# Performance work log

Hardware: AMD Instinct MI355X
Metric: run time of the kernel (lower is better)

## Reference

```python
import jax, jax.numpy as jnp
import numpy as np

B, T, C, H = 2, 2048, 2048, 16
DH = C // H  # 128
INNER = 4 * C  # 8192
EPS = 1e-5


def _ln(x, w, b):
    mu = jnp.mean(x, axis=-1, keepdims=True)
    var = jnp.mean((x - mu) ** 2, axis=-1, keepdims=True)
    return (x - mu) * jax.lax.rsqrt(var + EPS) * w + b


def _apply_rotary(x, cos, sin):
    # x: [B,H,T,DH]; cos/sin: [T,DH//2] broadcast over B,H
    x1 = x[..., ::2]
    x2 = x[..., 1::2]
    r = jnp.stack([x1 * cos - x2 * sin, x1 * sin + x2 * cos], axis=-1)
    return r.reshape(r.shape[:-2] + (-1,))


def setup_inputs() -> dict:
    key = jax.random.key(0)
    ks = jax.random.split(key, 8)
    std = 0.02
    x = jax.random.normal(ks[0], (B, T, C), dtype=jnp.float32)
    # RoPE tables
    inv_freq = 1.0 / (10000.0 ** (np.arange(0, DH, 2, dtype=np.float32) / DH))
    ang = np.arange(T, dtype=np.float32)[:, None] * inv_freq[None, :]  # [T, DH//2]
    cos = jnp.asarray(np.cos(ang))
    sin = jnp.asarray(np.sin(ang))
    return {
        "x": x,
        "cos": cos,
        "sin": sin,
        "ln1_w": jnp.ones((C,), jnp.float32),
        "ln1_b": jnp.zeros((C,), jnp.float32),
        "ln2_w": jnp.ones((C,), jnp.float32),
        "ln2_b": jnp.zeros((C,), jnp.float32),
        "W_qkv": jax.random.normal(ks[1], (C, 3 * C), jnp.float32) * std,
        "W_o": jax.random.normal(ks[2], (C, C), jnp.float32) * std,
        "W1": jax.random.normal(ks[3], (C, INNER), jnp.float32) * std,
        "W2": jax.random.normal(ks[4], (C, INNER), jnp.float32) * std,
        "W3": jax.random.normal(ks[5], (INNER, C), jnp.float32) * std,
    }


def reference(x, cos, sin, ln1_w, ln1_b, ln2_w, ln2_b, W_qkv, W_o, W1, W2, W3):
    # --- attention sub-block (pre-LN) ---
    a = _ln(x, ln1_w, ln1_b)
    qkv = a @ W_qkv  # [B,T,3C]
    q, k, v = jnp.split(qkv, 3, axis=-1)
    q = q.reshape(B, T, H, DH).transpose(0, 2, 1, 3)  # [B,H,T,DH]
    k = k.reshape(B, T, H, DH).transpose(0, 2, 1, 3)
    v = v.reshape(B, T, H, DH).transpose(0, 2, 1, 3)
    q = _apply_rotary(q, cos, sin)
    k = _apply_rotary(k, cos, sin)
    scores = jnp.einsum("bhtd,bhsd->bhts", q, k) / jnp.sqrt(jnp.float32(DH))
    mask = jnp.triu(jnp.full((T, T), -jnp.inf, dtype=scores.dtype), k=1)
    scores = scores + mask
    attn = jax.nn.softmax(scores, axis=-1)
    y = jnp.einsum("bhts,bhsd->bhtd", attn, v)
    y = y.transpose(0, 2, 1, 3).reshape(B, T, C) @ W_o
    x = x + y
    # --- SwiGLU MLP sub-block (pre-LN) ---
    h = _ln(x, ln2_w, ln2_b)
    m = (jax.nn.silu(h @ W1) * (h @ W2)) @ W3
    return x + m
```

## Files before the change

kernel.cpp:

```cpp
#include <hip/hip_runtime.h>
#include <hip/hip_bf16.h>
#include <cstdint>

#define DEVINL __device__ __forceinline__

using f32x4  = __attribute__((ext_vector_type(4))) float;
using short8 = __attribute__((ext_vector_type(8))) short;
using short4v = __attribute__((ext_vector_type(4))) short;

DEVINL float bf2f(__hip_bfloat16 h){ return __bfloat162float(h); }
DEVINL __hip_bfloat16 f2bf(float f){ return __float2bfloat16(f); }
DEVINL short bfbits(float f){ __hip_bfloat16 h = __float2bfloat16(f); short s; __builtin_memcpy(&s, &h, 2); return s; }
DEVINL float sb2f(short s){ uint32_t u = ((uint32_t)(uint16_t)s) << 16; float f; __builtin_memcpy(&f, &u, 4); return f; }

DEVINL void gl_lds16(const void* g, void* l){
  __builtin_amdgcn_global_load_lds((const __attribute__((address_space(1))) void*)g,
                                   (__attribute__((address_space(3))) void*)l, 16, 0, 0);
}

__global__ __launch_bounds__(256) void wtrans(const float* __restrict__ src,
                                              __hip_bfloat16* __restrict__ dst,
                                              int R, int C){
  __shared__ float tile[32][33];
  const int tr0 = blockIdx.y*32, tc0 = blockIdx.x*32;
  const int t = threadIdx.x;
  const int lr = t >> 3, lc = (t & 7) * 4;
  float4 v = *(const float4*)(src + (size_t)(tr0+lr)*C + tc0 + lc);
  tile[lr][lc] = v.x; tile[lr][lc+1] = v.y; tile[lr][lc+2] = v.z; tile[lr][lc+3] = v.w;
  __syncthreads();
  short4v o;
  o[0] = bfbits(tile[lc+0][lr]);
  o[1] = bfbits(tile[lc+1][lr]);
  o[2] = bfbits(tile[lc+2][lr]);
  o[3] = bfbits(tile[lc+3][lr]);
  *(short4v*)(dst + (size_t)(tc0+lr)*R + tr0 + lc) = o;
}

__global__ __launch_bounds__(256) void ln_k(const float* __restrict__ x,
                                            const float* __restrict__ w,
                                            const float* __restrict__ bia,
                                            __hip_bfloat16* __restrict__ out){
  const int row = blockIdx.x, t = threadIdx.x;
  const float* xr = x + (size_t)row*2048;
  float4 v0 = *(const float4*)(xr + t*4);
  float4 v1 = *(const float4*)(xr + 1024 + t*4);
  float s  = v0.x+v0.y+v0.z+v0.w + v1.x+v1.y+v1.z+v1.w;
  float ss = v0.x*v0.x+v0.y*v0.y+v0.z*v0.z+v0.w*v0.w
           + v1.x*v1.x+v1.y*v1.y+v1.z*v1.z+v1.w*v1.w;
  #pragma unroll
  for (int o=1;o<64;o<<=1){ s += __shfl_xor(s,o); ss += __shfl_xor(ss,o); }
  __shared__ float red[8];
  const int wv = t>>6, ln = t&63;
  if (ln==0){ red[wv]=s; red[4+wv]=ss; }
  __syncthreads();
  s = red[0]+red[1]+red[2]+red[3]; ss = red[4]+red[5]+red[6]+red[7];
  const float mu = s*(1.f/2048.f);
  const float inv = rsqrtf(ss*(1.f/2048.f) - mu*mu + 1e-5f);
  {
    float4 wv4 = *(const float4*)(w + t*4);
    float4 bv4 = *(const float4*)(bia + t*4);
    short4v o;
    o[0]=bfbits((v0.x-mu)*inv*wv4.x + bv4.x);
    o[1]=bfbits((v0.y-mu)*inv*wv4.y + bv4.y);
    o[2]=bfbits((v0.z-mu)*inv*wv4.z + bv4.z);
    o[3]=bfbits((v0.w-mu)*inv*wv4.w + bv4.w);
    *(short4v*)(out + (size_t)row*2048 + t*4) = o;
  }
  {
    float4 wv4 = *(const float4*)(w + 1024 + t*4);
    float4 bv4 = *(const float4*)(bia + 1024 + t*4);
    short4v o;
    o[0]=bfbits((v1.x-mu)*inv*wv4.x + bv4.x);
    o[1]=bfbits((v1.y-mu)*inv*wv4.y + bv4.y);
    o[2]=bfbits((v1.z-mu)*inv*wv4.z + bv4.z);
    o[3]=bfbits((v1.w-mu)*inv*wv4.w + bv4.w);
    *(short4v*)(out + (size_t)row*2048 + 1024 + t*4) = o;
  }
}

template<int EPI, int BM>
__global__ __launch_bounds__(512, 2) void gemmp(
    const __hip_bfloat16* __restrict__ A,
    const __hip_bfloat16* __restrict__ Bt,
    __hip_bfloat16* __restrict__ Cb,
    float* __restrict__ Cf,
    const float* __restrict__ resid,
    const __hip_bfloat16* __restrict__ emul,
    int M, int N, int K, int NTN)
{
  constexpr int MF    = BM/32;
  constexpr int LA    = BM/128;
  constexpr int ABY   = BM*64;
  constexpr int TILEB = ABY + 16384;
  extern __shared__ char smem[];
  const int tid = threadIdx.x, lane = tid & 63, wave = tid >> 6;
  const int l15 = lane & 15, l4 = lane >> 4;
  const int wm = wave >> 2, wn = wave & 3;

  const int nwg = gridDim.x;
  const int id  = blockIdx.x;
  const int swz = (id & 7) * (nwg >> 3) + (id >> 3);
  const int by = swz / NTN, bx = swz % NTN;
  const int row0 = by * BM, col0 = bx * 256;

  const __hip_bfloat16* srcA[LA]; int dstA[LA];
  #pragma unroll
  for (int g = 0; g < LA; ++g){
    const int c = g*512 + tid, r = c >> 2, s = c & 3;
    const int kbyte = (s*16) ^ (((r >> 1) & 3) << 4);
    srcA[g] = A + (size_t)(row0 + r)*K + (kbyte >> 1);
    dstA[g] = c*16;
  }
  const __hip_bfloat16* srcB[2]; int dstB[2];
  #pragma unroll
  for (int g = 0; g < 2; ++g){
    const int c = g*512 + tid, r = c >> 2, s = c & 3;
    const int kbyte = (s*16) ^ (((r >> 1) & 3) << 4);
    srcB[g] = Bt + (size_t)(col0 + r)*K + (kbyte >> 1);
    dstB[g] = c*16;
  }
  auto STAGE = [&](int bi, int kt){
    char* base = smem + bi*TILEB;
    #pragma unroll
    for (int g = 0; g < LA; ++g) gl_lds16(srcA[g] + kt*32, base + dstA[g]);
    #pragma unroll
    for (int g = 0; g < 2; ++g)  gl_lds16(srcB[g] + kt*32, base + ABY + dstB[g]);
  };

  const int rmask = ((l15 >> 1) & 3) << 4;
  int offA[MF], offB[4];
  #pragma unroll
  for (int m = 0; m < MF; ++m){
    const int r = wm*(BM/2) + m*16 + l15;
    offA[m] = r*64 + ((l4*16) ^ rmask);
  }
  #pragma unroll
  for (int n = 0; n < 4; ++n){
    const int r = wn*64 + n*16 + l15;
    offB[n] = r*64 + ((l4*16) ^ rmask);
  }

  f32x4 acc[MF][4] = {};
  const int NT = K >> 5;

  STAGE(0, 0); STAGE(1, 1); STAGE(2, 2);
  __builtin_amdgcn_sched_barrier(0);
  if constexpr (BM == 256) asm volatile("s_waitcnt vmcnt(8)" ::: "memory");
  else                     asm volatile("s_waitcnt vmcnt(6)" ::: "memory");
  __builtin_amdgcn_s_barrier();
  __builtin_amdgcn_sched_barrier(0);

  for (int t = 0; t < NT; ++t){
    const char* base = smem + (t & 3)*TILEB;
    if (t + 3 < NT) STAGE((t + 3) & 3, t + 3);
    short8 a[MF], b[4];
    #pragma unroll
    for (int m = 0; m < MF; ++m) a[m] = *(const short8*)(base + offA[m]);
    #pragma unroll
    for (int n = 0; n < 4; ++n)  b[n] = *(const short8*)(base + ABY + offB[n]);
    __builtin_amdgcn_s_setprio(1);
    #pragma unroll
    for (int m = 0; m < MF; ++m)
      #pragma unroll
      for (int n = 0; n < 4; ++n)
        acc[m][n] = __builtin_amdgcn_mfma_f32_16x16x32_bf16(a[m], b[n], acc[m][n], 0, 0, 0);
    __builtin_amdgcn_s_setprio(0);
    if (t + 3 < NT){
      if constexpr (BM == 256) asm volatile("s_waitcnt vmcnt(8)" ::: "memory");
      else                     asm volatile("s_waitcnt vmcnt(6)" ::: "memory");
    } else if (t + 2 < NT){
      if constexpr (BM == 256) asm volatile("s_waitcnt vmcnt(4)" ::: "memory");
      else                     asm volatile("s_waitcnt vmcnt(3)" ::: "memory");
    } else {
      asm volatile("s_waitcnt vmcnt(0)" ::: "memory");
    }
    __builtin_amdgcn_s_barrier();
    __builtin_amdgcn_sched_barrier(0);
  }

  #pragma unroll
  for (int m = 0; m < MF; ++m){
    const int r0 = row0 + wm*(BM/2) + m*16 + l4*4;
    #pragma unroll
    for (int n = 0; n < 4; ++n){
      const int c = col0 + wn*64 + n*16 + l15;
      #pragma unroll
      for (int j = 0; j < 4; ++j){
        const size_t idx = (size_t)(r0 + j)*N + c;
        const float v = acc[m][n][j];
        if constexpr (EPI == 1)      Cf[idx] = v + resid[idx];
        else if constexpr (EPI == 2) Cb[idx] = f2bf(v / (1.f + __expf(-v)));
        else if constexpr (EPI == 3) Cb[idx] = f2bf(v * bf2f(emul[idx]));
        else                         Cb[idx] = f2bf(v);
      }
    }
  }
}

__global__ __launch_bounds__(512, 2) void gemmf(
    const __hip_bfloat16* __restrict__ A,
    const __hip_bfloat16* __restrict__ B1t,
    const __hip_bfloat16* __restrict__ B2t,
    __hip_bfloat16* __restrict__ Cb,
    int M, int N, int K, int NTN)
{
  constexpr int ABY   = 16384;
  constexpr int TILEB = ABY + 16384;
  extern __shared__ char smem[];
  const int tid = threadIdx.x, lane = tid & 63, wave = tid >> 6;
  const int l15 = lane & 15, l4 = lane >> 4;
  const int wm = wave >> 2, wn = wave & 3;

  const int nwg = gridDim.x;
  const int id  = blockIdx.x;
  const int swz = (id & 7) * (nwg >> 3) + (id >> 3);
  const int by = swz / NTN, bx = swz % NTN;
  const int row0 = by * 256, col0 = bx * 128;

  const __hip_bfloat16* srcA[2]; int dstA[2];
  #pragma unroll
  for (int g = 0; g < 2; ++g){
    const int c = g*512 + tid, r = c >> 2, s = c & 3;
    const int kbyte = (s*16) ^ (((r >> 1) & 3) << 4);
    srcA[g] = A + (size_t)(row0 + r)*K + (kbyte >> 1);
    dstA[g] = c*16;
  }
  const __hip_bfloat16* srcB[2]; int dstB[2];
  #pragma unroll
  for (int g = 0; g < 2; ++g){
    const int c = g*512 + tid, r = c >> 2, s = c & 3;
    const int kbyte = (s*16) ^ (((r >> 1) & 3) << 4);
    const __hip_bfloat16* base = (r < 128) ? (B1t + (size_t)(col0 + r)*K)
                                           : (B2t + (size_t)(col0 + r - 128)*K);
    srcB[g] = base + (kbyte >> 1);
    dstB[g] = c*16;
  }
  auto STAGE = [&](int bi, int kt){
    char* base = smem + bi*TILEB;
    #pragma unroll
    for (int g = 0; g < 2; ++g) gl_lds16(srcA[g] + kt*32, base + dstA[g]);
    #pragma unroll
    for (int g = 0; g < 2; ++g) gl_lds16(srcB[g] + kt*32, base + ABY + dstB[g]);
  };

  const int rmask = ((l15 >> 1) & 3) << 4;
  int offA[8], offB[2][2];
  #pragma unroll
  for (int m = 0; m < 8; ++m){
    const int r = wm*128 + m*16 + l15;
    offA[m] = r*64 + ((l4*16) ^ rmask);
  }
  #pragma unroll
  for (int g = 0; g < 2; ++g)
    #pragma unroll
    for (int nf = 0; nf < 2; ++nf){
      const int r = g*128 + wn*32 + nf*16 + l15;
      offB[g][nf] = r*64 + ((l4*16) ^ rmask);
    }

  f32x4 acc[8][2][2] = {};
  const int NT = K >> 5;

  STAGE(0, 0); STAGE(1, 1); STAGE(2, 2);
  __builtin_amdgcn_sched_barrier(0);
  asm volatile("s_waitcnt vmcnt(8)" ::: "memory");
  __builtin_amdgcn_s_barrier();
  __builtin_amdgcn_sched_barrier(0);

  for (int t = 0; t < NT; ++t){
    const char* base = smem + (t & 3)*TILEB;
    if (t + 3 < NT) STAGE((t + 3) & 3, t + 3);
    short8 a[8], b[2][2];
    #pragma unroll
    for (int m = 0; m < 8; ++m) a[m] = *(const short8*)(base + offA[m]);
    #pragma unroll
    for (int g = 0; g < 2; ++g)
      #pragma unroll
      for (int nf = 0; nf < 2; ++nf) b[g][nf] = *(const short8*)(base + ABY + offB[g][nf]);
    __builtin_amdgcn_s_setprio(1);
    #pragma unroll
    for (int m = 0; m < 8; ++m)
      #pragma unroll
      for (int g = 0; g < 2; ++g)
        #pragma unroll
        for (int nf = 0; nf < 2; ++nf)
          acc[m][g][nf] = __builtin_amdgcn_mfma_f32_16x16x32_bf16(a[m], b[g][nf], acc[m][g][nf], 0, 0, 0);
    __builtin_amdgcn_s_setprio(0);
    if (t + 3 < NT)      asm volatile("s_waitcnt vmcnt(8)" ::: "memory");
    else if (t + 2 < NT) asm volatile("s_waitcnt vmcnt(4)" ::: "memory");
    else                 asm volatile("s_waitcnt vmcnt(0)" ::: "memory");
    __builtin_amdgcn_s_barrier();
    __builtin_amdgcn_sched_barrier(0);
  }

  #pragma unroll
  for (int m = 0; m < 8; ++m){
    const int r0 = row0 + wm*128 + m*16 + l4*4;
    #pragma unroll
    for (int nf = 0; nf < 2; ++nf){
      const int c = col0 + wn*32 + nf*16 + l15;
      #pragma unroll
      for (int j = 0; j < 4; ++j){
        const float h1 = acc[m][0][nf][j];
        const float h2 = acc[m][1][nf][j];
        Cb[(size_t)(r0 + j)*N + c] = f2bf((h1 / (1.f + __expf(-h1))) * h2);
      }
    }
  }
}

__global__ __launch_bounds__(256) void ropepack(
    const __hip_bfloat16* __restrict__ qkv, const float* __restrict__ cosT, const float* __restrict__ sinT,
    __hip_bfloat16* __restrict__ Qo, __hip_bfloat16* __restrict__ Ko, __hip_bfloat16* __restrict__ Vo)
{
  __shared__ short vt[128][72];
  const int bh = blockIdx.y, b = bh>>4, h = bh&15;
  const int t0 = blockIdx.x*64, tid = threadIdx.x;
  const int tr = tid>>2, q4 = tid&3;
  const int tg = t0 + tr;
  const __hip_bfloat16* base = qkv + ((size_t)(b*2048 + tg))*6144 + h*128;
  const int pp0 = q4*16;
  float cs[16], sn[16];
  #pragma unroll
  for (int i=0;i<4;i++){
    float4 c4 = *(const float4*)(cosT + (size_t)tg*64 + pp0 + i*4);
    float4 s4 = *(const float4*)(sinT + (size_t)tg*64 + pp0 + i*4);
    cs[i*4+0]=c4.x; cs[i*4+1]=c4.y; cs[i*4+2]=c4.z; cs[i*4+3]=c4.w;
    sn[i*4+0]=s4.x; sn[i*4+1]=s4.y; sn[i*4+2]=s4.z; sn[i*4+3]=s4.w;
  }
  #pragma unroll
  for (int qk=0; qk<2; ++qk){
    const __hip_bfloat16* src = base + qk*2048;
    __hip_bfloat16* dst = (qk==0 ? Qo : Ko) + ((size_t)bh*2048 + tg)*128 + pp0*2;
    short8 ov[4];
    short* o = (short*)ov;
    #pragma unroll
    for (int i=0;i<4;i++){
      short8 v = *(const short8*)(src + pp0*2 + i*8);
      #pragma unroll
      for (int j=0;j<4;j++){
        float xe = sb2f(v[2*j]), xo = sb2f(v[2*j+1]);
        float c = cs[4*i+j], s = sn[4*i+j];
        o[8*i+2*j]   = bfbits(xe*c - xo*s);
        o[8*i+2*j+1] = bfbits(xe*s + xo*c);
      }
    }
    #pragma unroll
    for (int i=0;i<4;i++) *(short8*)(dst + i*8) = ov[i];
  }
  const __hip_bfloat16* vsrc = base + 4096;
  const int vc0 = q4*32;
  #pragma unroll
  for (int i=0;i<4;i++){
    short8 v = *(const short8*)(vsrc + vc0 + i*8);
    #pragma unroll
    for (int j=0;j<8;j++) vt[vc0+i*8+j][tr] = v[j];
  }
  __syncthreads();
  const int d = tid>>1, th0 = (tid&1)*32;
  __hip_bfloat16* vdst = Vo + ((size_t)bh*128 + d)*2048 + t0 + th0;
  #pragma unroll
  for (int i=0;i<4;i++)
    *(short8*)(vdst + i*8) = *(const short8*)(&vt[d][th0 + i*8]);
}

__global__ __launch_bounds__(512, 2) void attn_k(
    const __hip_bfloat16* __restrict__ Q,
    const __hip_bfloat16* __restrict__ K,
    const __hip_bfloat16* __restrict__ Vt,
    __hip_bfloat16* __restrict__ Y)
{
  extern __shared__ char lds[];
  const int bh = blockIdx.x, b = bh>>4, h = bh&15;
  const int by = blockIdx.y;
  const int qtA = 15 - 2*by, qtB = 2*by;
  const int tid = threadIdx.x, lane = tid&63, wave = tid>>6;
  const int qt = (wave < 4) ? qtA : qtB;
  const int qbase = qt*128 + (wave&3)*32;
  const int qmax = (qtA > qtB) ? qtA : qtB;
  const int nsteps = 2*qmax + 2;
  const __hip_bfloat16* Qh = Q + (size_t)bh*2048*128;
  const __hip_bfloat16* Kh = K + (size_t)bh*2048*128;
  const __hip_bfloat16* Vh = Vt + (size_t)bh*128*2048;
  char* plbase = lds + 65536 + wave*4608;
  const int l15 = lane & 15, l4 = lane >> 4;
  const int swzm = (l15 & 7) << 4;

  const int krA = tid >> 4;  const int kjA = (tid & 15) * 16;
  const size_t ksrcA = (size_t)krA*128 + ((kjA ^ ((krA & 7) << 4)) >> 1);
  const size_t ksrcB = (size_t)(krA+32)*128 + ((kjA ^ ((krA & 7) << 4)) >> 1);
  const int vrA = tid >> 3;  const int vjA = (tid & 7) * 16;
  const size_t vsrcA = (size_t)vrA*2048 + ((vjA ^ ((vrA & 7) << 4)) >> 1);
  const size_t vsrcB = (size_t)(vrA+64)*2048 + ((vjA ^ ((vrA & 7) << 4)) >> 1);
  auto STAGE = [&](int buf, int kv0){
    char* kb = lds + buf*16384;
    char* vb = lds + 32768 + buf*16384;
    gl_lds16(Kh + (size_t)kv0*128 + ksrcA, kb + tid*16);
    gl_lds16(Kh + (size_t)kv0*128 + ksrcB, kb + 8192 + tid*16);
    gl_lds16(Vh + kv0 + vsrcA, vb + tid*16);
    gl_lds16(Vh + kv0 + vsrcB, vb + 8192 + tid*16);
  };

  short8 qf[2][4];
  #pragma unroll
  for (int m=0;m<2;m++)
    #pragma unroll
    for (int kc=0;kc<4;kc++)
      qf[m][kc] = *(const short8*)(Qh + (size_t)(qbase + m*16 + l15)*128 + kc*32 + l4*8);

  short8 of;
  #pragma unroll
  for (int i=0;i<8;i++) of[i] = (l15==0) ? (short)0x3F80 : (short)0;

  f32x4 accO[2][9] = {};
  float mrow[2][4];
  #pragma unroll
  for (int m=0;m<2;m++)
    #pragma unroll
    for (int j=0;j<4;j++) mrow[m][j] = -1e30f;
  const float scale = 0.08838834764831845f;

  STAGE(0, 0);
  STAGE(1, 64);
  __builtin_amdgcn_sched_barrier(0);
  asm volatile("s_waitcnt vmcnt(4)" ::: "memory");
  __builtin_amdgcn_s_barrier();
  __builtin_amdgcn_sched_barrier(0);

  for (int s = 0; s < nsteps; ++s){
    const int kv0 = s*64;
    const char* kb = lds + (s&1)*16384;
    const char* vb = lds + 32768 + (s&1)*16384;
    if (kv0 <= qbase){
      const bool diag = (kv0 + 64 > qbase);
      const int kvrel = kv0 - qbase;
      f32x4 sc[2][4] = {};
      #pragma unroll
      for (int n=0;n<4;n++){
        short8 kf[4];
        #pragma unroll
        for (int kc=0;kc<4;kc++)
          kf[kc] = *(const short8*)(kb + (n*16 + l15)*256 + ((kc*64 + l4*16) ^ swzm));
        #pragma unroll
        for (int m=0;m<2;m++)
          #pragma unroll
          for (int kc=0;kc<4;kc++)
            sc[m][n] = __builtin_amdgcn_mfma_f32_16x16x32_bf16(qf[m][kc], kf[kc], sc[m][n], 0,0,0);
      }
      float alpha_[2][4];
      #pragma unroll
      for (int m=0;m<2;m++)
        #pragma unroll
        for (int j=0;j<4;j++){
          const int qr = 16*m + 4*l4 + j;
          float a[4];
          #pragma unroll
          for (int n=0;n<4;n++){
            a[n] = sc[m][n][j]*scale;
            if (diag && (kvrel + n*16 + l15 > qr)) a[n] = -1e30f;
          }
          float mx = fmaxf(fmaxf(a[0],a[1]), fmaxf(a[2],a[3]));
          #pragma unroll
          for (int o=1;o<16;o<<=1) mx = fmaxf(mx, __shfl_xor(mx, o));
          const float mn = fmaxf(mrow[m][j], mx);
          const float al = __expf(mrow[m][j] - mn);
          mrow[m][j] = mn;
          alpha_[m][j] = al;
          __hip_bfloat16* pr = (__hip_bfloat16*)(plbase + qr*144) + l15;
          #pragma unroll
          for (int n=0;n<4;n++) pr[n*16] = f2bf(__expf(a[n] - mn));
        }
      #pragma unroll
      for (int m=0;m<2;m++)
        #pragma unroll
        for (int db=0;db<9;db++)
          #pragma unroll
          for (int j=0;j<4;j++)
            accO[m][db][j] *= alpha_[m][j];
      asm volatile("s_waitcnt lgkmcnt(0)" ::: "memory");
      __builtin_amdgcn_sched_barrier(0);
      short8 pa[2][2];
      #pragma unroll
      for (int m=0;m<2;m++)
        #pragma unroll
        for (int ks=0;ks<2;ks++)
          pa[m][ks] = *(const short8*)(plbase + (m*16 + l15)*144 + ks*64 + l4*16);
      #pragma unroll
      for (int db=0;db<8;db++){
        #pragma unroll
        for (int ks=0;ks<2;ks++){
          short8 vf = *(const short8*)(vb + (db*16 + l15)*128 + ((ks*64 + l4*16) ^ swzm));
          #pragma unroll
          for (int m=0;m<2;m++)
            accO[m][db] = __builtin_amdgcn_mfma_f32_16x16x32_bf16(pa[m][ks], vf, accO[m][db], 0,0,0);
        }
      }
      #pragma unroll
      for (int ks=0;ks<2;ks++)
        #pragma unroll
        for (int m=0;m<2;m++)
          accO[m][8] = __builtin_amdgcn_mfma_f32_16x16x32_bf16(pa[m][ks], of, accO[m][8], 0,0,0);
    }
    __builtin_amdgcn_sched_barrier(0);
    __builtin_amdgcn_s_barrier();
    __builtin_amdgcn_sched_barrier(0);
    if (s + 2 < nsteps){
      STAGE(s&1, (s+2)*64);
      __builtin_amdgcn_sched_barrier(0);
      asm volatile("s_waitcnt vmcnt(4)" ::: "memory");
    } else {
      asm volatile("s_waitcnt vmcnt(0)" ::: "memory");
    }
    __builtin_amdgcn_s_barrier();
    __builtin_amdgcn_sched_barrier(0);
  }

  #pragma unroll
  for (int m=0;m<2;m++){
    float lr[4];
    #pragma unroll
    for (int j=0;j<4;j++) lr[j] = __shfl(accO[m][8][j], l4*16);
    #pragma unroll
    for (int db=0;db<8;db++)
      #pragma unroll
      for (int j=0;j<4;j++){
        const int tg = qbase + 16*m + 4*l4 + j;
        const int d  = 16*db + l15;
        Y[((size_t)b*2048 + tg)*2048 + h*128 + d] = f2bf(accO[m][db][j] / lr[j]);
      }
  }
}

extern "C" void kernel_launch(void* const* d_in, const int* in_sizes, int n_in,
                              void* d_out, int out_size, void* d_ws, size_t ws_size,
                              hipStream_t stream)
{
  const float* x    = (const float*)d_in[0];
  const float* cosT = (const float*)d_in[1];
  const float* sinT = (const float*)d_in[2];
  const float* ln1w = (const float*)d_in[3];
  const float* ln1b = (const float*)d_in[4];
  const float* ln2w = (const float*)d_in[5];
  const float* ln2b = (const float*)d_in[6];
  const float* Wqkv = (const float*)d_in[7];
  const float* Wo   = (const float*)d_in[8];
  const float* W1   = (const float*)d_in[9];
  const float* W2   = (const float*)d_in[10];
  const float* W3   = (const float*)d_in[11];
  float* out = (float*)d_out;

  if (ws_size < 150994944) return;
  char* ws = (char*)d_ws;
  __hip_bfloat16* WT    = (__hip_bfloat16*)(ws);
  __hip_bfloat16* W2T   = (__hip_bfloat16*)(ws + 33554432);
  __hip_bfloat16* WoT   = (__hip_bfloat16*)(ws + 50331648);
  __hip_bfloat16* abf   = (__hip_bfloat16*)(ws + 67108864);
  __hip_bfloat16* qkvb  = (__hip_bfloat16*)(ws + 83886080);
  __hip_bfloat16* sub   = (__hip_bfloat16*)(ws + 83886080);
  __hip_bfloat16* Qb    = (__hip_bfloat16*)(ws);
  __hip_bfloat16* Kb    = (__hip_bfloat16*)(ws + 16777216);
  __hip_bfloat16* Vtb   = (__hip_bfloat16*)(ws + 33554432);
  __hip_bfloat16* Yb    = (__hip_bfloat16*)(ws + 134217728);
  float*          x2    = out;

  hipFuncSetAttribute(reinterpret_cast<const void*>(&gemmp<4,128>),
                      hipFuncAttributeMaxDynamicSharedMemorySize, 98304);
  hipFuncSetAttribute(reinterpret_cast<const void*>(&gemmp<1,128>),
                      hipFuncAttributeMaxDynamicSharedMemorySize, 98304);
  hipFuncSetAttribute(reinterpret_cast<const void*>(&gemmf),
                      hipFuncAttributeMaxDynamicSharedMemorySize, 131072);
  hipFuncSetAttribute(reinterpret_cast<const void*>(&attn_k),
                      hipFuncAttributeMaxDynamicSharedMemorySize, 102400);

  ln_k<<<4096,256,0,stream>>>(x, ln1w, ln1b, abf);
  wtrans<<<dim3(192,64),256,0,stream>>>(Wqkv, WT, 2048, 6144);
  gemmp<4,128><<<768,512,98304,stream>>>(abf, WT, qkvb, nullptr, nullptr, nullptr, 4096, 6144, 2048, 24);
  ropepack<<<dim3(32,32),256,0,stream>>>(qkvb, cosT, sinT, Qb, Kb, Vtb);
  attn_k<<<dim3(32,8),512,102400,stream>>>(Qb, Kb, Vtb, Yb);
  wtrans<<<dim3(64,64),256,0,stream>>>(Wo, WoT, 2048, 2048);
  gemmp<1,128><<<256,512,98304,stream>>>(Yb, WoT, nullptr, x2, x, nullptr, 4096, 2048, 2048, 8);
  ln_k<<<4096,256,0,stream>>>(x2, ln2w, ln2b, abf);
  wtrans<<<dim3(256,64),256,0,stream>>>(W1, WT, 2048, 8192);
  wtrans<<<dim3(256,64),256,0,stream>>>(W2, W2T, 2048, 8192);
  gemmf<<<1024,512,131072,stream>>>(abf, WT, W2T, sub, 4096, 8192, 2048, 64);
  wtrans<<<dim3(64,256),256,0,stream>>>(W3, WT, 8192, 2048);
  gemmp<1,128><<<256,512,98304,stream>>>(sub, WT, nullptr, out, x2, nullptr, 4096, 2048, 8192, 8);
}
```

Measured before the change: 796.3 us.

## Split paired attention q-tiles into separate 256-thread blocks with single V buffer

The attention kernel previously launched 512-thread blocks that each processed a short and a long query tile together, so every wave looped over the longer tile's KV range. It now launches twice as many 256-thread blocks, one query tile each, so a block only iterates over its own causal range. The pipeline is reorganised: K stays double-buffered, V is single-buffered and loaded at the start of each step so that load overlaps the QK/softmax phase, and the shared-memory request drops accordingly. This adds an extra barrier and a full vmcnt drain per step, and removes the load balancing that pairing short and long tiles provided.

```diff
diff --git a/kernel.cpp b/kernel.cpp
--- a/kernel.cpp
+++ b/kernel.cpp
@@ -364,7 +364,7 @@
     *(short8*)(vdst + i*8) = *(const short8*)(&vt[d][th0 + i*8]);
 }
 
-__global__ __launch_bounds__(512, 2) void attn_k(
+__global__ __launch_bounds__(256, 2) void attn_k(
     const __hip_bfloat16* __restrict__ Q,
     const __hip_bfloat16* __restrict__ K,
     const __hip_bfloat16* __restrict__ Vt,
@@ -373,32 +373,39 @@
   extern __shared__ char lds[];
   const int bh = blockIdx.x, b = bh>>4, h = bh&15;
   const int by = blockIdx.y;
-  const int qtA = 15 - 2*by, qtB = 2*by;
+  const int qt = (by < 8) ? (15 - 2*by) : (2*(by - 8));
   const int tid = threadIdx.x, lane = tid&63, wave = tid>>6;
-  const int qt = (wave < 4) ? qtA : qtB;
-  const int qbase = qt*128 + (wave&3)*32;
-  const int qmax = (qtA > qtB) ? qtA : qtB;
-  const int nsteps = 2*qmax + 2;
+  const int qbase = qt*128 + wave*32;
+  const int nsteps = 2*qt + 2;
   const __hip_bfloat16* Qh = Q + (size_t)bh*2048*128;
   const __hip_bfloat16* Kh = K + (size_t)bh*2048*128;
   const __hip_bfloat16* Vh = Vt + (size_t)bh*128*2048;
-  char* plbase = lds + 65536 + wave*4608;
+  char* plbase = lds + 49152 + wave*4608;
   const int l15 = lane & 15, l4 = lane >> 4;
   const int swzm = (l15 & 7) << 4;
 
-  const int krA = tid >> 4;  const int kjA = (tid & 15) * 16;
-  const size_t ksrcA = (size_t)krA*128 + ((kjA ^ ((krA & 7) << 4)) >> 1);
-  const size_t ksrcB = (size_t)(krA+32)*128 + ((kjA ^ ((krA & 7) << 4)) >> 1);
-  const int vrA = tid >> 3;  const int vjA = (tid & 7) * 16;
-  const size_t vsrcA = (size_t)vrA*2048 + ((vjA ^ ((vrA & 7) << 4)) >> 1);
-  const size_t vsrcB = (size_t)(vrA+64)*2048 + ((vjA ^ ((vrA & 7) << 4)) >> 1);
-  auto STAGE = [&](int buf, int kv0){
-    char* kb = lds + buf*16384;
-    char* vb = lds + 32768 + buf*16384;
-    gl_lds16(Kh + (size_t)kv0*128 + ksrcA, kb + tid*16);
-    gl_lds16(Kh + (size_t)kv0*128 + ksrcB, kb + 8192 + tid*16);
-    gl_lds16(Vh + kv0 + vsrcA, vb + tid*16);
-    gl_lds16(Vh + kv0 + vsrcB, vb + 8192 + tid*16);
+  size_t ksrc[4], vsrc[4];
+  int cdst[4];
+  #pragma unroll
+  for (int i = 0; i < 4; ++i){
+    const int c = i*256 + tid;
+    const int kr = c >> 4, kslot = c & 15;
+    const int kcolb = (kslot*16) ^ ((kr & 7) << 4);
+    ksrc[i] = (size_t)kr*128 + (kcolb >> 1);
+    const int vr = c >> 3, vslot = c & 7;
+    const int vcolb = (vslot*16) ^ ((vr & 7) << 4);
+    vsrc[i] = (size_t)vr*2048 + (vcolb >> 1);
+    cdst[i] = c*16;
+  }
+  auto STK = [&](int buf, int kv0){
+    #pragma unroll
+    for (int i = 0; i < 4; ++i)
+      gl_lds16(Kh + (size_t)kv0*128 + ksrc[i], lds + buf*16384 + cdst[i]);
+  };
+  auto STV = [&](int kv0){
+    #pragma unroll
+    for (int i = 0; i < 4; ++i)
+      gl_lds16(Vh + kv0 + vsrc[i], lds + 32768 + cdst[i]);
   };
 
   short8 qf[2][4];
@@ -420,18 +427,23 @@
     for (int j=0;j<4;j++) mrow[m][j] = -1e30f;
   const float scale = 0.08838834764831845f;
 
-  STAGE(0, 0);
-  STAGE(1, 64);
+  STK(0, 0);
   __builtin_amdgcn_sched_barrier(0);
-  asm volatile("s_waitcnt vmcnt(4)" ::: "memory");
+  asm volatile("s_waitcnt vmcnt(0)" ::: "memory");
   __builtin_amdgcn_s_barrier();
   __builtin_amdgcn_sched_barrier(0);
 
   for (int s = 0; s < nsteps; ++s){
     const int kv0 = s*64;
     const char* kb = lds + (s&1)*16384;
-    const char* vb = lds + 32768 + (s&1)*16384;
-    if (kv0 <= qbase){
+    const char* vb = lds + 32768;
+    const bool act = (kv0 <= qbase);
+    const bool pfK = (s + 1 < nsteps);
+    STV(kv0);
+    if (pfK) STK((s+1)&1, kv0 + 64);
+    __builtin_amdgcn_sched_barrier(0);
+    float alpha_[2][4];
+    if (act){
       const bool diag = (kv0 + 64 > qbase);
       const int kvrel = kv0 - qbase;
       f32x4 sc[2][4] = {};
@@ -447,7 +459,6 @@
           for (int kc=0;kc<4;kc++)
             sc[m][n] = __builtin_amdgcn_mfma_f32_16x16x32_bf16(qf[m][kc], kf[kc], sc[m][n], 0,0,0);
       }
-      float alpha_[2][4];
       #pragma unroll
       for (int m=0;m<2;m++)
         #pragma unroll
@@ -479,6 +490,12 @@
             accO[m][db][j] *= alpha_[m][j];
       asm volatile("s_waitcnt lgkmcnt(0)" ::: "memory");
       __builtin_amdgcn_sched_barrier(0);
+    }
+    if (pfK) asm volatile("s_waitcnt vmcnt(4)" ::: "memory");
+    else     asm volatile("s_waitcnt vmcnt(0)" ::: "memory");
+    __builtin_amdgcn_s_barrier();
+    __builtin_amdgcn_sched_barrier(0);
+    if (act){
       short8 pa[2][2];
       #pragma unroll
       for (int m=0;m<2;m++)
@@ -502,15 +519,7 @@
           accO[m][8] = __builtin_amdgcn_mfma_f32_16x16x32_bf16(pa[m][ks], of, accO[m][8], 0,0,0);
     }
     __builtin_amdgcn_sched_barrier(0);
-    __builtin_amdgcn_s_barrier();
-    __builtin_amdgcn_sched_barrier(0);
-    if (s + 2 < nsteps){
-      STAGE(s&1, (s+2)*64);
-      __builtin_amdgcn_sched_barrier(0);
-      asm volatile("s_waitcnt vmcnt(4)" ::: "memory");
-    } else {
-      asm volatile("s_waitcnt vmcnt(0)" ::: "memory");
-    }
+    asm volatile("s_waitcnt vmcnt(0)" ::: "memory");
     __builtin_amdgcn_s_barrier();
     __builtin_amdgcn_sched_barrier(0);
   }
@@ -570,13 +579,13 @@
   hipFuncSetAttribute(reinterpret_cast<const void*>(&gemmf),
                       hipFuncAttributeMaxDynamicSharedMemorySize, 131072);
   hipFuncSetAttribute(reinterpret_cast<const void*>(&attn_k),
-                      hipFuncAttributeMaxDynamicSharedMemorySize, 102400);
+                      hipFuncAttributeMaxDynamicSharedMemorySize, 67584);
 
   ln_k<<<4096,256,0,stream>>>(x, ln1w, ln1b, abf);
   wtrans<<<dim3(192,64),256,0,stream>>>(Wqkv, WT, 2048, 6144);
   gemmp<4,128><<<768,512,98304,stream>>>(abf, WT, qkvb, nullptr, nullptr, nullptr, 4096, 6144, 2048, 24);
   ropepack<<<dim3(32,32),256,0,stream>>>(qkvb, cosT, sinT, Qb, Kb, Vtb);
-  attn_k<<<dim3(32,8),512,102400,stream>>>(Qb, Kb, Vtb, Yb);
+  attn_k<<<dim3(32,16),256,67584,stream>>>(Qb, Kb, Vtb, Yb);
   wtrans<<<dim3(64,64),256,0,stream>>>(Wo, WoT, 2048, 2048);
   gemmp<1,128><<<256,512,98304,stream>>>(Yb, WoT, nullptr, x2, x, nullptr, 4096, 2048, 2048, 8);
   ln_k<<<4096,256,0,stream>>>(x2, ln2w, ln2b, abf);
```

Measured after the change: 790.1 us. Within noise of the previous version (-0.8%).
